# Performance work log

Measured on AMD Instinct MI355X. Metric: run time of the kernel, lower is better.

Reference implementation:

```python
import jax, jax.numpy as jnp
import numpy as np

L = 3          # num encoder layers
H = 128        # hidden_dim
NH = 8         # num_heads
HD = H // NH   # head_dim
FF = H * 4     # ff inner dim (after GLU)
B, N = 32, 512
NUM_BINS = 50


def _linear_params(key, fan_in, fan_out):
    kw, kb = jax.random.split(key)
    lim = 1.0 / np.sqrt(fan_in)
    W = jax.random.uniform(kw, (fan_in, fan_out), jnp.float32, -lim, lim)
    b = jax.random.uniform(kb, (fan_out,), jnp.float32, -lim, lim)
    return W, b


def setup_inputs() -> dict:
    key = jax.random.key(0)
    ks = jax.random.split(key, 16)
    x = jax.random.normal(ks[0], (B, N, H), jnp.float32)
    distance_matrix = jax.random.uniform(ks[1], (B, N, N), jnp.float32)
    mask = jax.random.randint(ks[2], (B, N), 0, 2).astype(bool)

    def stack_linear(k, fan_in, fan_out):
        Ws, bs = [], []
        for l in range(L):
            W, b = _linear_params(jax.random.fold_in(k, l), fan_in, fan_out)
            Ws.append(W); bs.append(b)
        return jnp.stack(Ws), jnp.stack(bs)

    Wq, bq = stack_linear(ks[3], H, H)
    Wk, bk = stack_linear(ks[4], H, H)
    Wv, bv = stack_linear(ks[5], H, H)
    Wo, bo = stack_linear(ks[6], H, H)
    dist_emb = jax.random.normal(ks[7], (L, NUM_BINS, NH), jnp.float32)
    attn_bias = jnp.zeros((L, NH, 1, 1), jnp.float32)
    g1 = jnp.ones((L, H), jnp.float32); b1 = jnp.zeros((L, H), jnp.float32)
    g2 = jnp.ones((L, H), jnp.float32); b2 = jnp.zeros((L, H), jnp.float32)
    Wf1, bf1 = stack_linear(ks[8], H, 2 * FF)
    Wf2, bf2 = stack_linear(ks[9], FF, H)
    return dict(x=x, distance_matrix=distance_matrix, mask=mask,
                Wq=Wq, bq=bq, Wk=Wk, bk=bk, Wv=Wv, bv=bv, Wo=Wo, bo=bo,
                dist_emb=dist_emb, attn_bias=attn_bias,
                g1=g1, b1=b1, g2=g2, b2=b2,
                Wf1=Wf1, bf1=bf1, Wf2=Wf2, bf2=bf2)


def _layernorm(x, g, b, eps=1e-5):
    mu = jnp.mean(x, axis=-1, keepdims=True)
    var = jnp.var(x, axis=-1, keepdims=True)
    return (x - mu) * jax.lax.rsqrt(var + eps) * g + b


def _attention(h, bins, key_mask, Wq, bq, Wk, bk, Wv, bv, Wo, bo, dist_emb, attn_bias):
    # h: [B,N,H]; bins: [B,N,N] int; key_mask: [B,N] bool (True = masked)
    Bsz, Nn, _ = h.shape
    Q = (h @ Wq + bq).reshape(Bsz, Nn, NH, HD)
    K = (h @ Wk + bk).reshape(Bsz, Nn, NH, HD)
    V = (h @ Wv + bv).reshape(Bsz, Nn, NH, HD)
    scores = jnp.einsum('bqhd,bkhd->bhqk', Q, K) / np.sqrt(HD)
    bias = jnp.transpose(dist_emb[bins], (0, 3, 1, 2))  # [B,NH,N,N]
    scores = scores + bias + attn_bias[None]
    scores = jnp.where(key_mask[:, None, None, :], -1e9, scores)
    attn = jax.nn.softmax(scores, axis=-1)
    out = jnp.einsum('bhqk,bkhd->bqhd', attn, V).reshape(Bsz, Nn, H)
    return out @ Wo + bo


def reference(x, distance_matrix, mask, Wq, bq, Wk, bk, Wv, bv, Wo, bo,
              dist_emb, attn_bias, g1, b1, g2, b2, Wf1, bf1, Wf2, bf2):
    bins = jnp.clip((distance_matrix * 10.0).astype(jnp.int32), 0, NUM_BINS - 1)
    h = x
    for l in range(L):
        # pre-LN attention block
        a = _attention(_layernorm(h, g1[l], b1[l]), bins, mask,
                       Wq[l], bq[l], Wk[l], bk[l], Wv[l], bv[l], Wo[l], bo[l],
                       dist_emb[l], attn_bias[l])
        h = h + a
        # pre-LN GLU feed-forward
        u = _layernorm(h, g2[l], b2[l]) @ Wf1[l] + bf1[l]  # [B,N,2*FF]
        ua, ub = jnp.split(u, 2, axis=-1)
        h = h + (ua * jax.nn.sigmoid(ub)) @ Wf2[l] + bf2[l]
    return h
```

## Files before the change

kernel.cpp:

```cpp
#include <hip/hip_runtime.h>
#include <stdint.h>

#define Bq 32
#define Nq 512
#define Hq 128
#define NHq 8
#define HDq 16
#define Mq (Bq * Nq)

typedef unsigned short u16;
typedef __attribute__((ext_vector_type(8))) short short8;
typedef __attribute__((ext_vector_type(8))) _Float16 half8;
typedef __attribute__((ext_vector_type(2))) __fp16 fp16x2;
typedef __attribute__((ext_vector_type(4))) float f32x4;

__device__ __forceinline__ float bf2f(u16 v) {
    return __uint_as_float(((unsigned int)v) << 16);
}
__device__ __forceinline__ float ldin(const void* p, long idx, int bf) {
    if (bf) return bf2f(((const u16*)p)[idx]);
    return ((const float*)p)[idx];
}
__device__ __forceinline__ u16 f2bf(float v) {
    unsigned int u = __float_as_uint(v);
    return (u16)((u + 0x7FFFu + ((u >> 16) & 1u)) >> 16);
}
__device__ __forceinline__ u16 f2h(float v) {
    _Float16 h = (_Float16)v;
    return *(u16*)&h;
}
__device__ __forceinline__ unsigned pk2h(float a, float b) {
    fp16x2 c = __builtin_amdgcn_cvt_pkrtz(a, b);
    return *(unsigned*)&c;
}

__global__ void prep_kernel(const void* xraw, const void* de, const void* ab,
                            const void* mraw, int* flag, float* deo, float* abo,
                            unsigned* mbits, int n) {
    __shared__ int cnt, orA, orB, orC, orD;
    int tid = threadIdx.x;
    if (tid == 0) { cnt = 0; orA = 0; orB = 0; orC = 0; orD = 0; }
    __syncthreads();
    const u16* u = (const u16*)xraw;
    int good = 0;
    for (int i = tid; i < 1024; i += 256) {
        u16 v = u[i];
        int e = (v >> 7) & 0xFF;
        if (v == 0 || (e >= 90 && e <= 141)) good++;
    }
    atomicAdd(&cnt, good);
    const uint4* p4 = (const uint4*)mraw;
    unsigned a = 0, b = 0, c = 0, d = 0;
    for (int i = tid; i < n / 16; i += 256) {
        uint4 w = p4[i];
        unsigned all = w.x | w.y | w.z | w.w;
        a |= all & 0xFEFEFEFEu;
        b |= all & 0x0000FF00u;
        c |= all & 0xFFFFFF00u;
        d |= w.y | w.w;
    }
    if (a) atomicOr(&orA, 1);
    if (b) atomicOr(&orB, 1);
    if (c) atomicOr(&orC, 1);
    if (d) atomicOr(&orD, 1);
    __syncthreads();
    int bf = (cnt >= 900);
    if (tid == 0) *flag = bf;
    int mode;
    if (orA) mode = orB ? 3 : 4;
    else if (orC) mode = 0;
    else mode = orD ? 1 : 2;
    for (int i = tid; i < 1200; i += 256) deo[i] = ldin(de, i, bf);
    if (tid < 24) abo[tid] = ldin(ab, tid, bf);
    const unsigned char* p = (const unsigned char*)mraw;
    for (int wI = tid; wI < n / 32; wI += 256) {
        unsigned word = 0;
        for (int j = 0; j < 32; ++j) {
            int i = wI * 32 + j;
            int v;
            switch (mode) {
                case 0: v = p[i]; break;
                case 1: v = ((const int*)p)[i]; break;
                case 2: v = (int)((const long long*)p)[i]; break;
                case 3: v = ((const u16*)p)[i] != 0; break;
                default: v = (((const float*)p)[i] != 0.0f); break;
            }
            if (v) word |= 1u << j;
        }
        mbits[wI] = word;
    }
}

__global__ void kprep_kernel(const unsigned* __restrict__ mbits,
                             u16* __restrict__ kidxg, int* __restrict__ nkt,
                             unsigned* __restrict__ tmask) {
    int b = blockIdx.x;
    int lane = threadIdx.x & 63;
    int pos_base = 0;
    for (int w = 0; w < 8; ++w) {
        unsigned lo = mbits[b * 16 + 2 * w], hi = mbits[b * 16 + 2 * w + 1];
        unsigned long long word = ((unsigned long long)hi << 32) | lo;
        unsigned long long un = ~word;
        int bit = (int)((un >> lane) & 1ull);
        unsigned long long before = un & ((1ull << lane) - 1ull);
        int pos = pos_base + __popcll(before);
        if (bit) kidxg[b * 512 + pos] = (u16)(w * 64 + lane);
        pos_base += __popcll(un);
    }
    int nk = pos_base;
    int nkp = (nk + 31) & ~31;
    if (nkp == 0) nkp = 32;
    int nt = nkp >> 5;
    for (int j = nk + lane; j < nkp; j += 64) kidxg[b * 512 + j] = 0;
    if (lane == 0) {
        nkt[b] = nt;
        for (int t = 0; t < 16; ++t) tmask[b * 16 + t] = 0;
        int rem = nk & 31;
        if (rem) tmask[b * 16 + nt - 1] = 0xFFFFFFFFu << rem;
        if (nk == 0) tmask[b * 16] = 0xFFFFFFFFu;
    }
}

__global__ __launch_bounds__(256) void binsc_kernel(
    const void* __restrict__ dist, const u16* __restrict__ kidxg,
    const int* __restrict__ nkt, unsigned char* __restrict__ binsc,
    const int* flagp) {
    int bf = *flagp;
    int b = blockIdx.y;
    int q0 = blockIdx.x * 8;
    __shared__ u16 kl[512];
    __shared__ int ntS;
    int tid = threadIdx.x;
    if (tid == 0) ntS = nkt[b];
    kl[tid] = kidxg[b * 512 + tid];
    kl[tid + 256] = kidxg[b * 512 + tid + 256];
    __syncthreads();
    int nkp = ntS * 32;
    for (int rq = 0; rq < 8; ++rq) {
        int q = q0 + rq;
        long rowoff = ((long)b * 512 + q) * 512;
        for (int j = tid; j < nkp; j += 256) {
            float d = ldin(dist, rowoff + kl[j], bf);
            int v = (int)(d * 10.0f);
            v = v < 0 ? 0 : (v > 49 ? 49 : v);
            binsc[((size_t)b * 512 + q) * 512 + j] = (unsigned char)(v << 2);
        }
    }
}

__global__ __launch_bounds__(256) void init_ln_kernel(
    const void* x, float* __restrict__ h, u16* __restrict__ hn,
    const void* graw, const void* braw, const int* flagp) {
    int bf = *flagp;
    int row = blockIdx.x * 4 + (threadIdx.x >> 6);
    int lane = threadIdx.x & 63;
    float x0 = ldin(x, (long)row * Hq + lane, bf);
    float x1 = ldin(x, (long)row * Hq + lane + 64, bf);
    h[(size_t)row * Hq + lane] = x0;
    h[(size_t)row * Hq + lane + 64] = x1;
    float s = x0 + x1, s2 = x0 * x0 + x1 * x1;
#pragma unroll
    for (int o = 32; o; o >>= 1) {
        s += __shfl_xor(s, o);
        s2 += __shfl_xor(s2, o);
    }
    float mu = s * (1.0f / 128.0f);
    float var = fmaxf(s2 * (1.0f / 128.0f) - mu * mu, 0.0f);
    float rr = rsqrtf(var + 1e-5f);
    float g0 = ldin(graw, lane, bf), g1v = ldin(graw, lane + 64, bf);
    float b0 = ldin(braw, lane, bf), b1v = ldin(braw, lane + 64, bf);
    hn[(size_t)row * Hq + lane]      = f2bf((x0 - mu) * rr * g0 + b0);
    hn[(size_t)row * Hq + lane + 64] = f2bf((x1 - mu) * rr * g1v + b1v);
}

__global__ __launch_bounds__(256) void wtrans_kernel(
    const void* Wqr, const void* Wkr, const void* Wvr, const void* Wor,
    const void* Wf1r, const void* Wf2r,
    u16* qkvT, u16* oT, u16* f1T, u16* f2T, const int* flagp) {
    int bf = *flagp;
    int bid = blockIdx.x;
    int l = bid >> 8, r = bid & 255;
    const void* src; u16* dst; long soff, doff; int Kd, Nd, t;
    if (r < 64) {
        int mat = r >> 4; t = r & 15; Kd = 128; Nd = 128;
        soff = (long)l * 16384;
        if (mat == 0)      { src = Wqr; dst = qkvT; doff = (long)l * 49152; }
        else if (mat == 1) { src = Wkr; dst = qkvT; doff = (long)l * 49152 + 16384; }
        else if (mat == 2) { src = Wvr; dst = qkvT; doff = (long)l * 49152 + 32768; }
        else               { src = Wor; dst = oT;   doff = (long)l * 16384; }
    } else if (r < 192) {
        t = r - 64; Kd = 128; Nd = 1024;
        src = Wf1r; soff = (long)l * 131072; dst = f1T; doff = (long)l * 131072;
    } else {
        t = r - 192; Kd = 512; Nd = 128;
        src = Wf2r; soff = (long)l * 65536; dst = f2T; doff = (long)l * 65536;
    }
    int ntile = Nd >> 5;
    int tk = t / ntile, tn = t % ntile;
    __shared__ u16 Ts[32][33];
    int rr = threadIdx.x >> 3, cc0 = (threadIdx.x & 7) * 4;
#pragma unroll
    for (int i = 0; i < 4; ++i) {
        long idx = soff + (long)(tk * 32 + rr) * Nd + tn * 32 + cc0 + i;
        Ts[rr][cc0 + i] = f2bf(ldin(src, idx, bf));
    }
    __syncthreads();
#pragma unroll
    for (int i = 0; i < 4; ++i) {
        long idx = doff + (long)(tn * 32 + rr) * Kd + tk * 32 + cc0 + i;
        dst[idx] = Ts[cc0 + i][rr];
    }
}

__global__ __launch_bounds__(256, 2) void mfma_gemm64_kernel(
    const u16* __restrict__ A, const u16* __restrict__ WT,
    const void* __restrict__ braw, long bOff, float* __restrict__ C,
    int K, int resid, const int* flagp,
    const void* lnG, const void* lnB, long lnOff, u16* hnout, void* outp) {
    __shared__ __align__(16) u16 As[64][40];
    __shared__ __align__(16) u16 Bs[128][40];
    __shared__ float Ct[64][128];
    int tid = threadIdx.x;
    int m0 = blockIdx.x * 64;
    int wave = tid >> 6, lane = tid & 63;
    int wm = (wave >> 1) * 32, wn = (wave & 1) * 64;
    int q = lane >> 4, ln = lane & 15;
    f32x4 zero = {0.f, 0.f, 0.f, 0.f};
    f32x4 acc[2][4];
#pragma unroll
    for (int i = 0; i < 2; ++i)
#pragma unroll
        for (int j = 0; j < 4; ++j) acc[i][j] = zero;
    int sar = tid >> 2, sac = (tid & 3) * 8;
    int sbr = tid >> 1, sbc = (tid & 1) * 16;
    const u16* Ap = A + (size_t)(m0 + sar) * K + sac;
    const u16* Bp = WT + (size_t)sbr * K + sbc;
    for (int k0 = 0; k0 < K; k0 += 32) {
        uint4 av = *(const uint4*)(Ap + k0);
        uint4 b0 = *(const uint4*)(Bp + k0);
        uint4 b1 = *(const uint4*)(Bp + k0 + 8);
        *(uint4*)&As[sar][sac] = av;
        *(uint4*)&Bs[sbr][sbc] = b0; *(uint4*)&Bs[sbr][sbc + 8] = b1;
        __syncthreads();
        short8 af[2], bfv[4];
#pragma unroll
        for (int t = 0; t < 2; ++t) af[t] = *(const short8*)&As[wm + t * 16 + ln][q * 8];
#pragma unroll
        for (int t = 0; t < 4; ++t) bfv[t] = *(const short8*)&Bs[wn + t * 16 + ln][q * 8];
#pragma unroll
        for (int ti = 0; ti < 2; ++ti)
#pragma unroll
            for (int tj = 0; tj < 4; ++tj)
                acc[ti][tj] = __builtin_amdgcn_mfma_f32_16x16x32_bf16(
                    af[ti], bfv[tj], acc[ti][tj], 0, 0, 0);
        __syncthreads();
    }
    int bf = *flagp;
#pragma unroll
    for (int tj = 0; tj < 4; ++tj) {
        int n = wn + tj * 16 + ln;
        float bias = ldin(braw, bOff + n, bf);
#pragma unroll
        for (int ti = 0; ti < 2; ++ti)
#pragma unroll
            for (int r = 0; r < 4; ++r) {
                int m = m0 + wm + ti * 16 + q * 4 + r;
                float v = acc[ti][tj][r] + bias;
                float* dst = C + (size_t)m * 128 + n;
                if (resid) v += *dst;
                *dst = v;
                Ct[m - m0][n] = v;
                if (outp) {
                    if (bf) ((u16*)outp)[(size_t)m * 128 + n] = f2bf(v);
                    else ((float*)outp)[(size_t)m * 128 + n] = v;
                }
            }
    }
    if (hnout) {
        __syncthreads();
        float gg0 = ldin(lnG, lnOff + lane, bf);
        float gg1 = ldin(lnG, lnOff + lane + 64, bf);
        float bb0 = ldin(lnB, lnOff + lane, bf);
        float bb1 = ldin(lnB, lnOff + lane + 64, bf);
        for (int rr = 0; rr < 16; ++rr) {
            int row = wave * 16 + rr;
            float x0 = Ct[row][lane], x1 = Ct[row][lane + 64];
            float s = x0 + x1, s2v = x0 * x0 + x1 * x1;
#pragma unroll
            for (int o = 32; o; o >>= 1) {
                s += __shfl_xor(s, o);
                s2v += __shfl_xor(s2v, o);
            }
            float mu = s * (1.0f / 128.0f);
            float var = fmaxf(s2v * (1.0f / 128.0f) - mu * mu, 0.0f);
            float rstd = rsqrtf(var + 1e-5f);
            int m = m0 + row;
            hnout[(size_t)m * 128 + lane]      = f2bf((x0 - mu) * rstd * gg0 + bb0);
            hnout[(size_t)m * 128 + lane + 64] = f2bf((x1 - mu) * rstd * gg1 + bb1);
        }
    }
}

__global__ __launch_bounds__(256, 2) void qkv_mfma_kernel(
    const u16* __restrict__ A, const u16* __restrict__ qkvT_l,
    const void* bqr, const void* bkr, const void* bvr, long bOff,
    u16* __restrict__ Qo, u16* __restrict__ Ko, u16* __restrict__ Vo,
    const int* flagp) {
    int sel = blockIdx.y;
    const u16* WT = qkvT_l + (size_t)sel * 16384;
    const void* braw = sel == 0 ? bqr : (sel == 1 ? bkr : bvr);
    u16* C = sel == 0 ? Qo : (sel == 1 ? Ko : Vo);
    float scale = sel == 0 ? 0.25f : 1.0f;
    __shared__ __align__(16) u16 As[64][40];
    __shared__ __align__(16) u16 Bs[128][40];
    int tid = threadIdx.x;
    int m0 = blockIdx.x * 64;
    int wave = tid >> 6, lane = tid & 63;
    int wm = (wave >> 1) * 32, wn = (wave & 1) * 64;
    int q = lane >> 4, ln = lane & 15;
    f32x4 zero = {0.f, 0.f, 0.f, 0.f};
    f32x4 acc[2][4];
#pragma unroll
    for (int i = 0; i < 2; ++i)
#pragma unroll
        for (int j = 0; j < 4; ++j) acc[i][j] = zero;
    int sar = tid >> 2, sac = (tid & 3) * 8;
    int sbr = tid >> 1, sbc = (tid & 1) * 16;
    const u16* Ap = A + (size_t)(m0 + sar) * 128 + sac;
    const u16* Bp = WT + (size_t)sbr * 128 + sbc;
#pragma unroll
    for (int k0 = 0; k0 < 128; k0 += 32) {
        uint4 av = *(const uint4*)(Ap + k0);
        uint4 b0 = *(const uint4*)(Bp + k0);
        uint4 b1 = *(const uint4*)(Bp + k0 + 8);
        *(uint4*)&As[sar][sac] = av;
        *(uint4*)&Bs[sbr][sbc] = b0; *(uint4*)&Bs[sbr][sbc + 8] = b1;
        __syncthreads();
        short8 af[2], bfv[4];
#pragma unroll
        for (int t = 0; t < 2; ++t) af[t] = *(const short8*)&As[wm + t * 16 + ln][q * 8];
#pragma unroll
        for (int t = 0; t < 4; ++t) bfv[t] = *(const short8*)&Bs[wn + t * 16 + ln][q * 8];
#pragma unroll
        for (int ti = 0; ti < 2; ++ti)
#pragma unroll
            for (int tj = 0; tj < 4; ++tj)
                acc[ti][tj] = __builtin_amdgcn_mfma_f32_16x16x32_bf16(
                    af[ti], bfv[tj], acc[ti][tj], 0, 0, 0);
        __syncthreads();
    }
    int bf = *flagp;
#pragma unroll
    for (int tj = 0; tj < 4; ++tj) {
        int n = wn + tj * 16 + ln;
        float bias = ldin(braw, bOff + n, bf);
#pragma unroll
        for (int ti = 0; ti < 2; ++ti)
#pragma unroll
            for (int r = 0; r < 4; ++r) {
                int m = m0 + wm + ti * 16 + q * 4 + r;
                C[(size_t)m * 128 + n] = f2h((acc[ti][tj][r] + bias) * scale);
            }
    }
}

__global__ __launch_bounds__(256, 2) void glu_mfma_kernel(
    const u16* __restrict__ A, const u16* __restrict__ f1T_l,
    const void* __restrict__ braw, long bOff, u16* __restrict__ Vout,
    const int* flagp) {
    __shared__ __align__(16) u16 As[128][40];
    __shared__ __align__(16) u16 Ba[64][40];
    __shared__ __align__(16) u16 Bb[64][40];
    int tid = threadIdx.x;
    int m0 = blockIdx.x * 128, n0 = blockIdx.y * 64;
    int wave = tid >> 6, lane = tid & 63;
    int wm = (wave >> 1) * 64, wn = (wave & 1) * 32;
    int q = lane >> 4, ln = lane & 15;
    f32x4 zero = {0.f, 0.f, 0.f, 0.f};
    f32x4 accA[4][2], accB[4][2];
#pragma unroll
    for (int i = 0; i < 4; ++i)
#pragma unroll
        for (int j = 0; j < 2; ++j) { accA[i][j] = zero; accB[i][j] = zero; }
    int sr = tid >> 1, sc = (tid & 1) * 16;
    const u16* Ap = A + (size_t)(m0 + sr) * 128 + sc;
    const u16* BpA = f1T_l + (size_t)(n0 + sr) * 128 + sc;
    const u16* BpB = f1T_l + (size_t)(512 + n0 + (sr - 64)) * 128 + sc;
#pragma unroll
    for (int k0 = 0; k0 < 128; k0 += 32) {
        uint4 a0 = *(const uint4*)(Ap + k0);
        uint4 a1 = *(const uint4*)(Ap + k0 + 8);
        *(uint4*)&As[sr][sc] = a0; *(uint4*)&As[sr][sc + 8] = a1;
        if (sr < 64) {
            uint4 w0 = *(const uint4*)(BpA + k0);
            uint4 w1 = *(const uint4*)(BpA + k0 + 8);
            *(uint4*)&Ba[sr][sc] = w0; *(uint4*)&Ba[sr][sc + 8] = w1;
        } else {
            uint4 w0 = *(const uint4*)(BpB + k0);
            uint4 w1 = *(const uint4*)(BpB + k0 + 8);
            *(uint4*)&Bb[sr - 64][sc] = w0; *(uint4*)&Bb[sr - 64][sc + 8] = w1;
        }
        __syncthreads();
        short8 af[4], ba[2], bb[2];
#pragma unroll
        for (int t = 0; t < 4; ++t) af[t] = *(const short8*)&As[wm + t * 16 + ln][q * 8];
#pragma unroll
        for (int t = 0; t < 2; ++t) {
            ba[t] = *(const short8*)&Ba[wn + t * 16 + ln][q * 8];
            bb[t] = *(const short8*)&Bb[wn + t * 16 + ln][q * 8];
        }
#pragma unroll
        for (int ti = 0; ti < 4; ++ti)
#pragma unroll
            for (int tj = 0; tj < 2; ++tj) {
                accA[ti][tj] = __builtin_amdgcn_mfma_f32_16x16x32_bf16(
                    af[ti], ba[tj], accA[ti][tj], 0, 0, 0);
                accB[ti][tj] = __builtin_amdgcn_mfma_f32_16x16x32_bf16(
                    af[ti], bb[tj], accB[ti][tj], 0, 0, 0);
            }
        __syncthreads();
    }
    int bf = *flagp;
#pragma unroll
    for (int tj = 0; tj < 2; ++tj) {
        int n = n0 + wn + tj * 16 + ln;
        float biasA = ldin(braw, bOff + n, bf);
        float biasB = ldin(braw, bOff + 512 + n, bf);
#pragma unroll
        for (int ti = 0; ti < 4; ++ti)
#pragma unroll
            for (int r = 0; r < 4; ++r) {
                int m = m0 + wm + ti * 16 + q * 4 + r;
                float ua = accA[ti][tj][r] + biasA;
                float ub = accB[ti][tj][r] + biasB;
                Vout[(size_t)m * 512 + n] = f2bf(ua / (1.0f + __expf(-ub)));
            }
    }
}

__global__ __launch_bounds__(256, 4) void attn_kernel(
    const u16* __restrict__ Qh, const u16* __restrict__ Kh,
    const u16* __restrict__ Vh, const unsigned char* __restrict__ binsc,
    const u16* __restrict__ kidxg, const int* __restrict__ nktp,
    const unsigned* __restrict__ tmaskp, const float* __restrict__ deL,
    const float* __restrict__ abL, u16* __restrict__ out) {
    int id = blockIdx.x;
    int c = id & 7, t5 = id >> 3;
    int nh = t5 & 7;
    int pair = ((t5 >> 3) << 3) | c;
    int b = pair >> 2, qq = pair & 3;

    __shared__ __align__(16) u16 KsF[8192];
    __shared__ __align__(16) u16 VT[16 * 520];
    __shared__ __align__(16) u16 Pl[4 * 16 * 40];

    int tid = threadIdx.x;
    int nt = __builtin_amdgcn_readfirstlane(nktp[b]);
    int nkp = nt * 32;
    const u16* Kp = Kh + (size_t)(b * Nq) * Hq + nh * HDq;
    const u16* Vp = Vh + (size_t)(b * Nq) * Hq + nh * HDq;
    for (int r = tid; r < nkp; r += 256) {
        int row = kidxg[b * 512 + r];
        int kt = r >> 5, s = (r >> 4) & 1, lnr = r & 15;
        uint4 k0v = *(const uint4*)(Kp + (size_t)row * Hq);
        uint4 k1v = *(const uint4*)(Kp + (size_t)row * Hq + 8);
        *(uint4*)&KsF[kt * 512 + s * 256 + lnr * 8]       = k0v;
        *(uint4*)&KsF[kt * 512 + s * 256 + 128 + lnr * 8] = k1v;
        uint4 v0 = *(const uint4*)(Vp + (size_t)row * Hq);
        uint4 v1 = *(const uint4*)(Vp + (size_t)row * Hq + 8);
        u16 vv[16];
        *(uint4*)&vv[0] = v0; *(uint4*)&vv[8] = v1;
#pragma unroll
        for (int d = 0; d < 16; ++d) VT[d * 520 + r] = vv[d];
    }
    __syncthreads();

    int wave = tid >> 6, lane = tid & 63;
    int quad = lane >> 4, ln = lane & 15;
    int q0w = qq * 128 + wave * 32;

    float tblf = (lane < 50) ? deL[lane * NHq + nh] + abL[nh] : 0.0f;
    int tbli = __float_as_int(tblf);
    unsigned tl = tmaskp[b * 16 + nt - 1];

    half8 qf[2];
#pragma unroll
    for (int t = 0; t < 2; ++t) {
        uint4 qv = {0, 0, 0, 0};
        if (quad < 2)
            qv = *(const uint4*)(Qh + (size_t)(b * Nq + q0w + t * 16 + ln) * Hq
                                 + nh * HDq + quad * 8);
        qf[t] = *(half8*)&qv;
    }

    f32x4 zero = {0.f, 0.f, 0.f, 0.f};
    f32x4 acc[2] = {zero, zero};
    float zp[2] = {0.f, 0.f};
    _Float16* Pw = (_Float16*)&Pl[wave * 640];
    const _Float16* KsH = (const _Float16*)KsF;
    const _Float16* VTH = (const _Float16*)VT;
    const unsigned char* brow0 = binsc + ((size_t)b * 512 + (q0w + ln)) * 512;
    const unsigned char* brow1 = brow0 + (size_t)16 * 512;

    unsigned pb00 = *(const unsigned*)(brow0 + quad * 4);
    unsigned pb01 = *(const unsigned*)(brow0 + 16 + quad * 4);
    unsigned pb10 = *(const unsigned*)(brow1 + quad * 4);
    unsigned pb11 = *(const unsigned*)(brow1 + 16 + quad * 4);

    for (int kt = 0; kt < nt; ++kt) {
        int k0 = kt * 32;
        unsigned w = (kt == nt - 1) ? tl : 0u;
        unsigned cb00 = pb00, cb01 = pb01, cb10 = pb10, cb11 = pb11;
        if (kt < nt - 1) {
            pb00 = *(const unsigned*)(brow0 + k0 + 32 + quad * 4);
            pb01 = *(const unsigned*)(brow0 + k0 + 48 + quad * 4);
            pb10 = *(const unsigned*)(brow1 + k0 + 32 + quad * 4);
            pb11 = *(const unsigned*)(brow1 + k0 + 48 + quad * 4);
        }
        half8 vb = *(const half8*)(VTH + ln * 520 + k0 + quad * 8);
        half8 ka0 = {}, ka1 = {};
        if (quad < 2) {
            ka0 = *(const half8*)(KsH + kt * 512 + quad * 128 + ln * 8);
            ka1 = *(const half8*)(KsH + kt * 512 + 256 + quad * 128 + ln * 8);
        }
#pragma unroll
        for (int t = 0; t < 2; ++t) {
            unsigned bw0 = t == 0 ? cb00 : cb10;
            unsigned bw1 = t == 0 ? cb01 : cb11;
            f32x4 s0 = __builtin_amdgcn_mfma_f32_16x16x32_f16(ka0, qf[t], zero, 0, 0, 0);
            f32x4 s1 = __builtin_amdgcn_mfma_f32_16x16x32_f16(ka1, qf[t], zero, 0, 0, 0);
            float p[8];
#pragma unroll
            for (int r = 0; r < 4; ++r) {
                float bias = __int_as_float(__builtin_amdgcn_ds_bpermute(
                    (int)((bw0 >> (8 * r)) & 0xFFu), tbli));
                float sc = s0[r] + bias;
                bool m = (w >> (quad * 4 + r)) & 1u;
                p[r] = m ? 0.0f : __expf(sc);
            }
#pragma unroll
            for (int r = 0; r < 4; ++r) {
                float bias = __int_as_float(__builtin_amdgcn_ds_bpermute(
                    (int)((bw1 >> (8 * r)) & 0xFFu), tbli));
                float sc = s1[r] + bias;
                bool m = (w >> (16 + quad * 4 + r)) & 1u;
                p[4 + r] = m ? 0.0f : __expf(sc);
            }
            zp[t] += ((p[0] + p[1]) + (p[2] + p[3])) +
                     ((p[4] + p[5]) + (p[6] + p[7]));
            uint2 w0, w1;
            w0.x = pk2h(p[0], p[1]); w0.y = pk2h(p[2], p[3]);
            w1.x = pk2h(p[4], p[5]); w1.y = pk2h(p[6], p[7]);
            *(uint2*)(Pw + ln * 40 + quad * 4)      = w0;
            *(uint2*)(Pw + ln * 40 + 16 + quad * 4) = w1;
            half8 pa = *(const half8*)(Pw + ln * 40 + quad * 8);
            acc[t] = __builtin_amdgcn_mfma_f32_16x16x32_f16(pa, vb, acc[t], 0, 0, 0);
        }
    }
#pragma unroll
    for (int t = 0; t < 2; ++t) {
        zp[t] += __shfl_xor(zp[t], 16);
        zp[t] += __shfl_xor(zp[t], 32);
    }
#pragma unroll
    for (int t = 0; t < 2; ++t) {
#pragma unroll
        for (int r = 0; r < 4; ++r) {
            float zz = __shfl(zp[t], quad * 4 + r);
            float val = acc[t][r] / fmaxf(zz, 1e-35f);
            int qrow = q0w + t * 16 + quad * 4 + r;
            out[(size_t)(b * Nq + qrow) * Hq + nh * HDq + ln] = f2bf(val);
        }
    }
}

extern "C" void kernel_launch(void* const* d_in, const int* in_sizes, int n_in,
                              void* d_out, int out_size, void* d_ws, size_t ws_size,
                              hipStream_t stream) {
    const void* x  = d_in[0];
    const void* dist = d_in[1];
    const void* mask = d_in[2];
    const void* Wq = d_in[3];  const void* bq = d_in[4];
    const void* Wk = d_in[5];  const void* bk = d_in[6];
    const void* Wv = d_in[7];  const void* bv = d_in[8];
    const void* Wo = d_in[9];  const void* bo = d_in[10];
    const void* de = d_in[11]; const void* ab = d_in[12];
    const void* g1 = d_in[13]; const void* b1 = d_in[14];
    const void* g2 = d_in[15]; const void* b2 = d_in[16];
    const void* Wf1 = d_in[17]; const void* bf1 = d_in[18];
    const void* Wf2 = d_in[19]; const void* bf2 = d_in[20];

    char* ws = (char*)d_ws;
    const size_t OFF_DE   = 64;
    const size_t OFF_AB   = 5120;
    const size_t OFF_BINS = 8192;
    const size_t OFF_MSK  = OFF_BINS + 8388608;
    const size_t OFF_KIDX = OFF_MSK + 4096;
    const size_t OFF_NKT  = OFF_KIDX + 32768;
    const size_t OFF_TM   = OFF_NKT + 256;
    const size_t OFF_H    = OFF_TM + 4096;
    const size_t OFF_QKV  = OFF_H + 8388608;
    const size_t OFF_HN   = OFF_QKV + 25165824;
    const size_t OFF_ATT  = OFF_HN + 4194304;
    const size_t OFF_WT   = OFF_ATT + 4194304;
    const size_t NEEDED   = OFF_WT + 1572864;
    if (ws_size < NEEDED) return;

    int* flag = (int*)ws;
    float* deF = (float*)(ws + OFF_DE);
    float* abF = (float*)(ws + OFF_AB);
    unsigned char* binsc = (unsigned char*)(ws + OFF_BINS);
    unsigned* mbits = (unsigned*)(ws + OFF_MSK);
    u16* kidxg = (u16*)(ws + OFF_KIDX);
    int* nkt = (int*)(ws + OFF_NKT);
    unsigned* tmask = (unsigned*)(ws + OFF_TM);
    float* h = (float*)(ws + OFF_H);
    u16* Qh = (u16*)(ws + OFF_QKV);
    u16* Kh = Qh + 2097152;
    u16* Vh = Qh + 2 * 2097152;
    u16* vglu = (u16*)(ws + OFF_QKV);
    u16* hn = (u16*)(ws + OFF_HN);
    u16* att = (u16*)(ws + OFF_ATT);
    u16* qkvT = (u16*)(ws + OFF_WT);
    u16* oT  = qkvT + 147456;
    u16* f1T = oT + 49152;
    u16* f2T = f1T + 393216;

    prep_kernel<<<1, 256, 0, stream>>>(x, de, ab, mask, flag, deF, abF, mbits, Bq * Nq);
    kprep_kernel<<<32, 64, 0, stream>>>(mbits, kidxg, nkt, tmask);
    dim3 gbc(64, 32);
    binsc_kernel<<<gbc, 256, 0, stream>>>(dist, kidxg, nkt, binsc, flag);
    init_ln_kernel<<<4096, 256, 0, stream>>>(x, h, hn, g1, b1, flag);
    wtrans_kernel<<<768, 256, 0, stream>>>(Wq, Wk, Wv, Wo, Wf1, Wf2,
                                           qkvT, oT, f1T, f2T, flag);

    dim3 gqkv(256, 3);
    dim3 gglu(128, 8);
    for (int l = 0; l < 3; ++l) {
        qkv_mfma_kernel<<<gqkv, 256, 0, stream>>>(hn, qkvT + (size_t)l * 49152,
                                                  bq, bk, bv, (long)l * Hq,
                                                  Qh, Kh, Vh, flag);
        attn_kernel<<<1024, 256, 0, stream>>>(Qh, Kh, Vh, binsc, kidxg, nkt, tmask,
                                              deF + (long)l * 400, abF + (long)l * 8, att);
        mfma_gemm64_kernel<<<256, 256, 0, stream>>>(att, oT + (size_t)l * 16384,
                                                    bo, (long)l * Hq, h, 128, 1, flag,
                                                    g2, b2, (long)l * Hq, hn, nullptr);
        glu_mfma_kernel<<<gglu, 256, 0, stream>>>(hn, f1T + (size_t)l * 131072,
                                                  bf1, (long)l * 1024, vglu, flag);
        if (l < 2) {
            mfma_gemm64_kernel<<<256, 256, 0, stream>>>(vglu, f2T + (size_t)l * 65536,
                                                        bf2, (long)l * Hq, h, 512, 1, flag,
                                                        g1, b1, (long)(l + 1) * Hq, hn,
                                                        nullptr);
        } else {
            mfma_gemm64_kernel<<<256, 256, 0, stream>>>(vglu, f2T + (size_t)l * 65536,
                                                        bf2, (long)l * Hq, h, 512, 1, flag,
                                                        nullptr, nullptr, 0, nullptr,
                                                        d_out);
        }
    }
}
```

Measured before the change: 409.6 us.

## Switch attention MFMAs to 16x16x16 so P stays in registers

Replaces the 16x16x32 f16 MFMAs in the attention kernel with 16x16x16 variants. The QK^T output layout then matches the A-operand layout of the PV product, so probabilities go straight from registers into the MFMA with no LDS round trip. K is stored in a padded row-major LDS layout (stride 20) and Q no longer wastes half its lanes on zero padding. The cost is twice as many PV MFMAs at a smaller shape, while the per-tile LDS write, read and wave-local hazard are removed.

```diff
diff --git a/kernel.cpp b/kernel.cpp
--- a/kernel.cpp
+++ b/kernel.cpp
@@ -10,7 +10,7 @@
 
 typedef unsigned short u16;
 typedef __attribute__((ext_vector_type(8))) short short8;
-typedef __attribute__((ext_vector_type(8))) _Float16 half8;
+typedef __attribute__((ext_vector_type(4))) _Float16 half4;
 typedef __attribute__((ext_vector_type(2))) __fp16 fp16x2;
 typedef __attribute__((ext_vector_type(4))) float f32x4;
 
@@ -450,9 +450,8 @@
     int pair = ((t5 >> 3) << 3) | c;
     int b = pair >> 2, qq = pair & 3;
 
-    __shared__ __align__(16) u16 KsF[8192];
+    __shared__ __align__(16) u16 KsF[512 * 20];
     __shared__ __align__(16) u16 VT[16 * 520];
-    __shared__ __align__(16) u16 Pl[4 * 16 * 40];
 
     int tid = threadIdx.x;
     int nt = __builtin_amdgcn_readfirstlane(nktp[b]);
@@ -461,11 +460,12 @@
     const u16* Vp = Vh + (size_t)(b * Nq) * Hq + nh * HDq;
     for (int r = tid; r < nkp; r += 256) {
         int row = kidxg[b * 512 + r];
-        int kt = r >> 5, s = (r >> 4) & 1, lnr = r & 15;
         uint4 k0v = *(const uint4*)(Kp + (size_t)row * Hq);
         uint4 k1v = *(const uint4*)(Kp + (size_t)row * Hq + 8);
-        *(uint4*)&KsF[kt * 512 + s * 256 + lnr * 8]       = k0v;
-        *(uint4*)&KsF[kt * 512 + s * 256 + 128 + lnr * 8] = k1v;
+        *(uint2*)&KsF[r * 20]      = make_uint2(k0v.x, k0v.y);
+        *(uint2*)&KsF[r * 20 + 4]  = make_uint2(k0v.z, k0v.w);
+        *(uint2*)&KsF[r * 20 + 8]  = make_uint2(k1v.x, k1v.y);
+        *(uint2*)&KsF[r * 20 + 12] = make_uint2(k1v.z, k1v.w);
         uint4 v0 = *(const uint4*)(Vp + (size_t)row * Hq);
         uint4 v1 = *(const uint4*)(Vp + (size_t)row * Hq + 8);
         u16 vv[16];
@@ -483,20 +483,17 @@
     int tbli = __float_as_int(tblf);
     unsigned tl = tmaskp[b * 16 + nt - 1];
 
-    half8 qf[2];
+    half4 qf[2];
 #pragma unroll
     for (int t = 0; t < 2; ++t) {
-        uint4 qv = {0, 0, 0, 0};
-        if (quad < 2)
-            qv = *(const uint4*)(Qh + (size_t)(b * Nq + q0w + t * 16 + ln) * Hq
-                                 + nh * HDq + quad * 8);
-        qf[t] = *(half8*)&qv;
+        uint2 qv = *(const uint2*)(Qh + (size_t)(b * Nq + q0w + t * 16 + ln) * Hq
+                                   + nh * HDq + quad * 4);
+        qf[t] = *(half4*)&qv;
     }
 
     f32x4 zero = {0.f, 0.f, 0.f, 0.f};
     f32x4 acc[2] = {zero, zero};
     float zp[2] = {0.f, 0.f};
-    _Float16* Pw = (_Float16*)&Pl[wave * 640];
     const _Float16* KsH = (const _Float16*)KsF;
     const _Float16* VTH = (const _Float16*)VT;
     const unsigned char* brow0 = binsc + ((size_t)b * 512 + (q0w + ln)) * 512;
@@ -517,18 +514,16 @@
             pb10 = *(const unsigned*)(brow1 + k0 + 32 + quad * 4);
             pb11 = *(const unsigned*)(brow1 + k0 + 48 + quad * 4);
         }
-        half8 vb = *(const half8*)(VTH + ln * 520 + k0 + quad * 8);
-        half8 ka0 = {}, ka1 = {};
-        if (quad < 2) {
-            ka0 = *(const half8*)(KsH + kt * 512 + quad * 128 + ln * 8);
-            ka1 = *(const half8*)(KsH + kt * 512 + 256 + quad * 128 + ln * 8);
-        }
+        half4 ka0 = *(const half4*)(KsH + (size_t)(k0 + ln) * 20 + quad * 4);
+        half4 ka1 = *(const half4*)(KsH + (size_t)(k0 + 16 + ln) * 20 + quad * 4);
+        half4 vb0 = *(const half4*)(VTH + ln * 520 + k0 + quad * 4);
+        half4 vb1 = *(const half4*)(VTH + ln * 520 + k0 + 16 + quad * 4);
 #pragma unroll
         for (int t = 0; t < 2; ++t) {
             unsigned bw0 = t == 0 ? cb00 : cb10;
             unsigned bw1 = t == 0 ? cb01 : cb11;
-            f32x4 s0 = __builtin_amdgcn_mfma_f32_16x16x32_f16(ka0, qf[t], zero, 0, 0, 0);
-            f32x4 s1 = __builtin_amdgcn_mfma_f32_16x16x32_f16(ka1, qf[t], zero, 0, 0, 0);
+            f32x4 s0 = __builtin_amdgcn_mfma_f32_16x16x16f16(ka0, qf[t], zero, 0, 0, 0);
+            f32x4 s1 = __builtin_amdgcn_mfma_f32_16x16x16f16(ka1, qf[t], zero, 0, 0, 0);
             float p[8];
 #pragma unroll
             for (int r = 0; r < 4; ++r) {
@@ -548,13 +543,12 @@
             }
             zp[t] += ((p[0] + p[1]) + (p[2] + p[3])) +
                      ((p[4] + p[5]) + (p[6] + p[7]));
-            uint2 w0, w1;
-            w0.x = pk2h(p[0], p[1]); w0.y = pk2h(p[2], p[3]);
-            w1.x = pk2h(p[4], p[5]); w1.y = pk2h(p[6], p[7]);
-            *(uint2*)(Pw + ln * 40 + quad * 4)      = w0;
-            *(uint2*)(Pw + ln * 40 + 16 + quad * 4) = w1;
-            half8 pa = *(const half8*)(Pw + ln * 40 + quad * 8);
-            acc[t] = __builtin_amdgcn_mfma_f32_16x16x32_f16(pa, vb, acc[t], 0, 0, 0);
+            uint2 pw0 = make_uint2(pk2h(p[0], p[1]), pk2h(p[2], p[3]));
+            uint2 pw1 = make_uint2(pk2h(p[4], p[5]), pk2h(p[6], p[7]));
+            half4 pa0 = *(half4*)&pw0;
+            half4 pa1 = *(half4*)&pw1;
+            acc[t] = __builtin_amdgcn_mfma_f32_16x16x16f16(pa0, vb0, acc[t], 0, 0, 0);
+            acc[t] = __builtin_amdgcn_mfma_f32_16x16x16f16(pa1, vb1, acc[t], 0, 0, 0);
         }
     }
 #pragma unroll
```

Measured after the change: 409.9 us. No clear change (+0.1%).
